# Optimization experiments

Hardware: AMD Instinct MI355X
Metric: run time of the kernel (lower is better)

## Reference

```python
import jax, jax.numpy as jnp
import numpy as np

N, C, H, W = 2, 256, 128, 128      # batch, fin=fout=fmiddle, feature resolution
SNC, NH, HS = 35, 128, 256         # semantic_nc, nhidden, raw segmap resolution
EPS = 1e-5                          # BatchNorm eps


def _conv(x, w, b, pad):
    y = jax.lax.conv_general_dilated(x, w, (1, 1), [(pad, pad), (pad, pad)],
                                     dimension_numbers=('NCHW', 'OIHW', 'NCHW'))
    return y + b[None, :, None, None]


def _bn(x, g, b):
    # training-mode BatchNorm2d: biased batch stats over (N, H, W)
    m = x.mean(axis=(0, 2, 3), keepdims=True)
    v = ((x - m) ** 2).mean(axis=(0, 2, 3), keepdims=True)
    return (x - m) * jax.lax.rsqrt(v + EPS) * g[None, :, None, None] + b[None, :, None, None]


def _depth_conv(x, w):
    # per-pixel dynamic 3x3 depthwise conv: unfold + multiply + reduce
    n, c, h, ww = x.shape
    xp = jnp.pad(x, ((0, 0), (0, 0), (1, 1), (1, 1)))
    patches = jnp.stack([xp[:, :, i:i + h, j:j + ww]
                         for i in range(3) for j in range(3)], axis=2)  # (N,C,9,H,W)
    return jnp.sum(patches * w.reshape(n, c, 9, h, ww), axis=2)


def _lrelu(x):
    return jnp.where(x >= 0, x, 0.2 * x)


def _branch(segmap, w1, b1, w2, b2):
    return _conv(jax.nn.relu(_conv(segmap, w1, b1, 1)), w2, b2, 1)


def _forward(x, seg, gw1_w1, gw1_b1, gw1_w2, gw1_b2, gw2_w1, gw2_b1, gw2_w2, gw2_b2,
             se1_w1, se1_b1, se1_w2, se1_b2, se2_w1, se2_b1, se2_w2, se2_b2,
             conv1_w, conv1_b, conv3_w, conv3_b, bn1_g, bn1_b, bn2_g, bn2_b):
    # F.interpolate(seg, size=(H, W), mode='nearest')
    ih = (jnp.arange(H) * seg.shape[2]) // H
    iw = (jnp.arange(W) * seg.shape[3]) // W
    segmap = seg[:, :, ih][:, :, :, iw]
    cw1 = _branch(segmap, gw1_w1, gw1_b1, gw1_w2, gw1_b2)                  # (N, C*9, H, W)
    cw2 = _branch(segmap, gw2_w1, gw2_b1, gw2_w2, gw2_b2)                  # (N, C*9, H, W)
    sw1 = jax.nn.sigmoid(_branch(segmap, se1_w1, se1_b1, se1_w2, se1_b2))  # (N, C, H, W)
    sw2 = jax.nn.sigmoid(_branch(segmap, se2_w1, se2_b1, se2_w2, se2_b2))  # (N, C, H, W)
    dx = _bn(x, bn1_g, bn1_b)
    dx = _depth_conv(dx, cw1)
    dx = _conv(dx, conv1_w, conv1_b, 0)
    dx = _lrelu(dx * sw1)
    dx = _bn(dx, bn2_g, bn2_b)
    dx = _depth_conv(dx, cw2)
    dx = _conv(dx, conv3_w, conv3_b, 0)
    dx = _lrelu(dx * sw2)
    return x + dx  # fin == fout -> identity shortcut


def setup_inputs() -> dict:
    key = jax.random.key(0)
    ks = jax.random.split(key, 22)
    def rn(i, shape, s=0.05):
        return jax.random.normal(ks[i], shape, jnp.float32) * s
    return {
        'x': jax.random.normal(ks[0], (N, C, H, W), jnp.float32),
        'seg': jax.random.uniform(ks[1], (N, SNC, HS, HS), jnp.float32),
        'gw1_w1': rn(2, (NH, SNC, 3, 3)), 'gw1_b1': rn(3, (NH,)),
        'gw1_w2': rn(4, (C * 9, NH, 3, 3)), 'gw1_b2': rn(5, (C * 9,)),
        'gw2_w1': rn(6, (NH, SNC, 3, 3)), 'gw2_b1': rn(7, (NH,)),
        'gw2_w2': rn(8, (C * 9, NH, 3, 3)), 'gw2_b2': rn(9, (C * 9,)),
        'se1_w1': rn(10, (NH, SNC, 3, 3)), 'se1_b1': rn(11, (NH,)),
        'se1_w2': rn(12, (C, NH, 3, 3)), 'se1_b2': rn(13, (C,)),
        'se2_w1': rn(14, (NH, SNC, 3, 3)), 'se2_b1': rn(15, (NH,)),
        'se2_w2': rn(16, (C, NH, 3, 3)), 'se2_b2': rn(17, (C,)),
        'conv1_w': rn(18, (C, C, 1, 1)), 'conv1_b': rn(19, (C,)),
        'conv3_w': rn(20, (C, C, 1, 1)), 'conv3_b': rn(21, (C,)),
        'bn1_g': jnp.ones((C,), jnp.float32), 'bn1_b': jnp.zeros((C,), jnp.float32),
        'bn2_g': jnp.ones((C,), jnp.float32), 'bn2_b': jnp.zeros((C,), jnp.float32),
    }


def reference(x, seg, gw1_w1, gw1_b1, gw1_w2, gw1_b2, gw2_w1, gw2_b1, gw2_w2, gw2_b2,
              se1_w1, se1_b1, se1_w2, se1_b2, se2_w1, se2_b1, se2_w2, se2_b2,
              conv1_w, conv1_b, conv3_w, conv3_b, bn1_g, bn1_b, bn2_g, bn2_b):
    return _forward(x, seg, gw1_w1, gw1_b1, gw1_w2, gw1_b2, gw2_w1, gw2_b1, gw2_w2, gw2_b2,
                    se1_w1, se1_b1, se1_w2, se1_b2, se2_w1, se2_b1, se2_w2, se2_b2,
                    conv1_w, conv1_b, conv3_w, conv3_b, bn1_g, bn1_b, bn2_g, bn2_b)
```

## Files before the change

kernel.cpp:

```cpp
#include <hip/hip_runtime.h>
#include <hip/hip_bf16.h>

typedef unsigned short u16;
typedef unsigned int u32;
typedef __attribute__((ext_vector_type(8))) short bf16x8;
typedef __attribute__((ext_vector_type(4))) float f32x4;
typedef __attribute__((address_space(3))) u32 lds_u32;
typedef const __attribute__((address_space(1))) u32 glb_u32;

#define H_ 128
#define W_ 128
#define PX 16384
#define PH 130

__device__ __forceinline__ float b2f(u16 h){ u32 u = ((u32)h)<<16; return __uint_as_float(u); }
__device__ __forceinline__ u16 f2b(float f){
  u32 u = __float_as_uint(f);
  u32 r = (u + 0x7fffu + ((u>>16)&1u)) >> 16;
  return (u16)r;
}
__device__ __forceinline__ float ldv(const void* p, long i, int m){
  return m ? ((const float*)p)[i] : b2f(((const u16*)p)[i]);
}
__device__ __forceinline__ void gload16(const u16* g, u16* l){
  __builtin_amdgcn_global_load_lds((glb_u32*)g, (lds_u32*)l, 16, 0, 0);
}

__global__ void k_detect(const u32* __restrict__ xw, u32* __restrict__ flag){
  __shared__ int cnt[256];
  const int t = threadIdx.x;
  int c = 0;
  #pragma unroll
  for (int i=0;i<4;i++){
    const u32 w = xw[t*4+i];
    const u32 e = ((w & 0xFFFFu) >> 7) & 0xFF;
    if (e >= 90 && e <= 140) c++;
  }
  cnt[t] = c; __syncthreads();
  for (int s=128;s>0;s>>=1){ if (t<s) cnt[t]+=cnt[t+s]; __syncthreads(); }
  if (t==0) flag[0] = (cnt[0] < 512) ? 1u : 0u;
}

__global__ void k_zpad(u16* __restrict__ h1t){
  const int p = blockIdx.x;
  u16* base = h1t + (long)p*2163200L;
  const int t = threadIdx.x;
  const int4 z = make_int4(0,0,0,0);
  for (int idx=t; idx<8256; idx+=256){
    long off;
    if (idx < 2080)       off = (long)idx*8;
    else if (idx < 4160)  off = 2146560L + (long)(idx-2080)*8;
    else if (idx < 6208){ const int r = 1 + (idx-4160)/16, w = (idx-4160)%16;
                          off = (long)r*16640 + w*8; }
    else {                const int r = 1 + (idx-6208)/16, w = (idx-6208)%16;
                          off = (long)r*16640 + 16512 + w*8; }
    *(int4*)(base + off) = z;
  }
}

template<int CIN, int NTAPS, int EPI>
__global__ __launch_bounds__(256, 2)
void k_convgemm(const u16* __restrict__ inp, const u16* __restrict__ wp,
                const u16* __restrict__ bias, const u16* __restrict__ swp,
                u16* __restrict__ outp, int nbco,
                long in_br, long w_br, int bias_br, long out_br,
                long in_n, int in_row, int in_x0,
                long out_n, long out_y, int out_px, int out_x0,
                long sw_n, int sw_y,
                const void* __restrict__ xres, const u32* __restrict__ flagp,
                void* __restrict__ outF, float* __restrict__ partp)
{
  __shared__ u16 ls[17408];
  u16* lsA = ls;
  u16* lsB = ls + 8192;

  const int bx  = blockIdx.x;
  const int y   = (NTAPS==9) ? (((bx&7)<<4) | (bx>>3)) : bx;
  const int br  = blockIdx.y / nbco;
  const int cb  = blockIdx.y - br*nbco;
  const int n   = blockIdx.z;
  const int tid = threadIdx.x;
  const int wave = tid >> 6, lane = tid & 63;
  const int l16 = lane & 15, lg = lane >> 4;
  const int chw = (wave >> 1) * 64;
  const int phw = (wave & 1) * 64;

  const u16* inb   = inp + (long)br*in_br + (long)n*in_n + in_x0 + (long)y*in_row;
  const u16* wb    = wp  + (long)br*w_br + (long)cb*128*(NTAPS*CIN);
  const u16* biasb = bias + (long)br*bias_br + cb*128;
  u16* outb = outp + (long)br*out_br + (long)n*out_n + out_x0 + (long)y*out_y;

  f32x4 acc[4][4];
  #pragma unroll
  for (int m=0;m<4;m++)
    #pragma unroll
    for (int q=0;q<4;q++) acc[m][q] = (f32x4){0.f,0.f,0.f,0.f};

  const int NSTEP = NTAPS*(CIN/64);
  for (int step=0; step<NSTEP; ++step){
    const int tap = step/(CIN/64);
    const int k0  = (step - tap*(CIN/64))*64;
    const int dy = (NTAPS==1)?0:(tap/3-1);
    const int dx = (NTAPS==1)?0:(tap%3-1);
    const u16* wsrc = wb  + tap*CIN + k0;
    const u16* bsrc = inb + (long)dy*in_row + dx*CIN + k0;
    #pragma unroll
    for (int i=0;i<4;i++){
      const int idx = (wave*4+i)*64 + lane;
      const int r = idx>>3, c = idx&7;
      const int cc = c ^ (r&7);
      gload16(wsrc + (long)r*(NTAPS*CIN) + cc*8, lsA + (wave*4+i)*512);
    }
    #pragma unroll
    for (int i=0;i<4;i++){
      const int idx = (wave*4+i)*64 + lane;
      const int r = idx>>3, c = idx&7;
      const int cc = c ^ (r&7);
      gload16(bsrc + (long)r*CIN + cc*8, lsB + (wave*4+i)*512);
    }
    __syncthreads();
    #pragma unroll
    for (int kk=0;kk<2;kk++){
      bf16x8 af[4], bfr[4];
      const int kc = kk*4 + lg;
      #pragma unroll
      for (int m=0;m<4;m++){
        const int r = chw + m*16 + l16;
        af[m] = *(const bf16x8*)(lsA + r*64 + ((kc ^ (r&7))<<3));
      }
      #pragma unroll
      for (int q=0;q<4;q++){
        const int r = phw + q*16 + l16;
        bfr[q] = *(const bf16x8*)(lsB + r*64 + ((kc ^ (r&7))<<3));
      }
      #pragma unroll
      for (int m=0;m<4;m++)
        #pragma unroll
        for (int q=0;q<4;q++)
          acc[m][q] = __builtin_amdgcn_mfma_f32_16x16x32_bf16(af[m], bfr[q], acc[m][q], 0,0,0);
    }
    __syncthreads();
  }

  #pragma unroll
  for (int m=0;m<4;m++){
    const int co = chw + m*16 + lg*4;
    const ushort4 bb = *(const ushort4*)(biasb + co);
    const float bv0=b2f(bb.x), bv1=b2f(bb.y), bv2=b2f(bb.z), bv3=b2f(bb.w);
    #pragma unroll
    for (int q=0;q<4;q++){
      const int px = phw + q*16 + l16;
      float v0 = acc[m][q][0] + bv0;
      float v1 = acc[m][q][1] + bv1;
      float v2 = acc[m][q][2] + bv2;
      float v3 = acc[m][q][3] + bv3;
      if (EPI==1){
        v0=fmaxf(v0,0.f); v1=fmaxf(v1,0.f); v2=fmaxf(v2,0.f); v3=fmaxf(v3,0.f);
      } else if (EPI==2){
        v0 = 1.f/(1.f+__expf(-v0)); v1 = 1.f/(1.f+__expf(-v1));
        v2 = 1.f/(1.f+__expf(-v2)); v3 = 1.f/(1.f+__expf(-v3));
      } else if (EPI==3 || EPI==4){
        const ushort4 sv = *(const ushort4*)(swp + (long)n*sw_n + (long)y*sw_y + (long)px*256 + cb*128 + co);
        v0 *= b2f(sv.x); v1 *= b2f(sv.y); v2 *= b2f(sv.z); v3 *= b2f(sv.w);
        v0 = v0>=0.f? v0 : 0.2f*v0;  v1 = v1>=0.f? v1 : 0.2f*v1;
        v2 = v2>=0.f? v2 : 0.2f*v2;  v3 = v3>=0.f? v3 : 0.2f*v3;
      }
      ushort4 ov; ov.x=f2b(v0); ov.y=f2b(v1); ov.z=f2b(v2); ov.w=f2b(v3);
      *(ushort4*)(ls + px*136 + co) = ov;
    }
  }
  __syncthreads();
  if (EPI == 4){
    const int m2 = (int)flagp[0];
    const int co = tid>>1, hf2 = tid&1;
    const long xoff = (((long)n*256 + cb*128 + co)*H_ + y)*W_ + hf2*64;
    const u16* lrow = ls + (hf2*64)*136 + co;
    if (m2){
      const float* xf = (const float*)xres;
      float* of = (float*)outF;
      #pragma unroll
      for (int i=0;i<16;i++){
        const float4 xv = *(const float4*)(xf + xoff + i*4);
        float4 ov;
        ov.x = xv.x + b2f(lrow[(i*4+0)*136]);
        ov.y = xv.y + b2f(lrow[(i*4+1)*136]);
        ov.z = xv.z + b2f(lrow[(i*4+2)*136]);
        ov.w = xv.w + b2f(lrow[(i*4+3)*136]);
        *(float4*)(of + xoff + i*4) = ov;
      }
    } else {
      const u16* xu = (const u16*)xres;
      u16* ou = (u16*)outF;
      #pragma unroll
      for (int i=0;i<8;i++){
        const bf16x8 xv = *(const bf16x8*)(xu + xoff + i*8);
        bf16x8 ov;
        #pragma unroll
        for (int e=0;e<8;e++)
          ov[e] = (short)f2b(b2f((u16)xv[e]) + b2f(lrow[(i*8+e)*136]));
        *(bf16x8*)(ou + xoff + i*8) = ov;
      }
    }
  } else {
    const int row = tid>>1, hf = tid&1;
    u16* og = outb + (long)row*out_px + cb*128 + hf*64;
    #pragma unroll
    for (int i=0;i<8;i++)
      *(int4*)(og + i*8) = *(const int4*)(ls + row*136 + hf*64 + i*8);
    if (EPI == 3){
      if (tid < 128){
        const int co = tid;
        float s = 0.f, q = 0.f;
        for (int px=0; px<128; ++px){
          const float v = b2f(ls[px*136 + co]);
          s += v; q += v*v;
        }
        float* o = partp + (((long)n*128 + y)*256 + cb*128 + co)*2;
        o[0] = s; o[1] = q;
      }
    }
  }
}

__global__ __launch_bounds__(256, 2)
void k_convdw(const u16* __restrict__ h1,
              const u16* __restrict__ wp,
              const u16* __restrict__ bp,
              const u16* __restrict__ xh,
              const float2* __restrict__ ss,
              u16* __restrict__ dd)
{
  __shared__ u16 ls[19008];
  u16* lsA = ls;
  u16* lsB = ls + 9216;

  const int bx = blockIdx.x, mt = blockIdx.y, n = blockIdx.z;
  const int y = ((bx&7)<<4) | (bx>>3);
  const int tid = threadIdx.x;
  const int wave = tid >> 6, lane = tid & 63;
  const int l16 = lane & 15, lg = lane >> 4;
  const int wn = wave * 32;

  const u16* wb = wp + (long)mt*144*1152;

  f32x4 acc[9][2];
  #pragma unroll
  for (int m=0;m<9;m++){ acc[m][0]=(f32x4){0,0,0,0}; acc[m][1]=(f32x4){0,0,0,0}; }

  for (int s=0; s<18; ++s){
    const int tap = s >> 1;
    const int k0  = (s & 1) * 64;
    const int dy = tap/3 - 1, dx = tap%3 - 1;
    const u16* wsrc = wb + tap*128 + k0;
    const u16* bsrc = h1 + (((long)n*PH + (y+dy+1))*PH + (dx+1))*128 + k0;
    #pragma unroll
    for (int i=0;i<4;i++){
      const int g = i*256 + tid;
      const int r = g>>3, c = g&7, sp = c ^ (r&7);
      gload16(wsrc + (long)r*1152 + sp*8, lsA + g*8);
    }
    if (tid < 128){
      const int g = 1024 + tid;
      const int r = g>>3, c = g&7, sp = c ^ (r&7);
      gload16(wsrc + (long)r*1152 + sp*8, lsA + g*8);
    }
    #pragma unroll
    for (int i=0;i<4;i++){
      const int g = i*256 + tid;
      const int p = g>>3, c = g&7, sp = c ^ (p&7);
      gload16(bsrc + (long)p*128 + sp*8, lsB + g*8);
    }
    __syncthreads();
    #pragma unroll
    for (int kk=0;kk<2;kk++){
      const int kc = kk*4 + lg;
      bf16x8 bfr[2];
      #pragma unroll
      for (int q=0;q<2;q++){
        const int rb = wn + q*16 + l16;
        bfr[q] = *(const bf16x8*)(lsB + rb*64 + ((kc ^ (rb&7))<<3));
      }
      #pragma unroll
      for (int m=0;m<9;m++){
        const int ra = m*16 + l16;
        const bf16x8 a = *(const bf16x8*)(lsA + ra*64 + ((kc ^ (ra&7))<<3));
        acc[m][0] = __builtin_amdgcn_mfma_f32_16x16x32_bf16(a, bfr[0], acc[m][0], 0,0,0);
        acc[m][1] = __builtin_amdgcn_mfma_f32_16x16x32_bf16(a, bfr[1], acc[m][1], 0,0,0);
      }
    }
    __syncthreads();
  }

  u16* ct = ls;
  #pragma unroll
  for (int m=0;m<9;m++){
    const int r0 = m*16 + lg*4;
    const ushort4 bb = *(const ushort4*)(bp + mt*144 + r0);
    const float bv0=b2f(bb.x), bv1=b2f(bb.y), bv2=b2f(bb.z), bv3=b2f(bb.w);
    #pragma unroll
    for (int q=0;q<2;q++){
      const int px = wn + q*16 + l16;
      ct[(r0+0)*132 + px] = f2b(acc[m][q][0] + bv0);
      ct[(r0+1)*132 + px] = f2b(acc[m][q][1] + bv1);
      ct[(r0+2)*132 + px] = f2b(acc[m][q][2] + bv2);
      ct[(r0+3)*132 + px] = f2b(acc[m][q][3] + bv3);
    }
  }
  __syncthreads();

  const int cl = tid & 15;
  const int c  = mt*16 + cl;
  const float2 sc = ss[c];
  const int xg = tid >> 4;
  #pragma unroll
  for (int i=0;i<8;i++){
    const int x = i*16 + xg;
    float a = 0.f;
    #pragma unroll
    for (int k=0;k<9;k++){
      const int ddy = k/3-1, ddx = k%3-1;
      const int gy = y+ddy, gx = x+ddx;
      if ((unsigned)gy < 128u && (unsigned)gx < 128u){
        const float xv = b2f(xh[(((long)n*PH + (gy+1))*PH + (gx+1))*256 + c]);
        const float w  = b2f(ct[(cl*9+k)*132 + x]);
        a += (xv*sc.x + sc.y) * w;
      }
    }
    dd[(((long)n*PX) + (long)y*W_ + x)*256 + c] = f2b(a);
  }
}

__global__ void k_bnstat2(const float* __restrict__ part, const void* __restrict__ g,
                          const void* __restrict__ b, const u32* __restrict__ flag,
                          float2* __restrict__ st)
{
  const int m = (int)flag[0];
  const int c = threadIdx.x;
  float s=0.f,q=0.f;
  for (int w=0;w<256;w++){ s += part[((long)w*256+c)*2]; q += part[((long)w*256+c)*2+1]; }
  const float mean = s*(1.f/32768.f);
  float v = q*(1.f/32768.f) - mean*mean;
  v = fmaxf(v, 0.f);
  const float sc = ldv(g,c,m) / sqrtf(v + 1e-5f);
  st[c] = make_float2(sc, ldv(b,c,m) - mean*sc);
}

__global__ void k_prep_w1(const void* a,const void* b,const void* c,const void* d,
                          const void* ba,const void* bb,const void* bc,const void* bd,
                          const u32* flag, u16* w1p, u16* bp1)
{
  const int m = (int)flag[0];
  const int idx = blockIdx.x*256 + threadIdx.x;
  if (idx < 294912){
    const int ci = idx & 63, r = (idx>>6)%9, co = (idx/576)%128, brn = idx/73728;
    const void* w = brn==0?a:brn==1?b:brn==2?c:d;
    u16 v = 0;
    if (ci < 35) v = f2b(ldv(w, ((long)co*35 + ci)*9 + r, m));
    w1p[idx] = v;
  }
  if (idx < 512){
    const int brn = idx>>7, co = idx&127;
    const void* bb2 = brn==0?ba:brn==1?bb:brn==2?bc:bd;
    bp1[idx] = f2b(ldv(bb2, co, m));
  }
}

__global__ void k_prep_gw(const void* __restrict__ w2, const void* __restrict__ b2,
                          const u32* __restrict__ flag,
                          u16* __restrict__ w2p, u16* __restrict__ bp)
{
  __shared__ u16 lt[2304];
  const int m = (int)flag[0];
  const int b = blockIdx.x;
  const int t = threadIdx.x;
  #pragma unroll
  for (int i=0;i<9;i++){
    const int g = i*256 + t;
    const long src = (long)b*2304 + g;
    const int lco = g/1152, rem = g - lco*1152;
    const int ci = rem/9, tap = rem - ci*9;
    lt[lco*1152 + tap*128 + ci] = f2b(ldv(w2, src, m));
  }
  __syncthreads();
  #pragma unroll
  for (int i=0;i<9;i++){
    const int g = i*256 + t;
    w2p[(long)b*2304 + g] = lt[g];
  }
  if (b < 9){
    const int bi = b*256 + t;
    if (bi < 2304) bp[bi] = f2b(ldv(b2, bi, m));
  }
}

__global__ void k_prep_se(const void* wa, const void* wb, const void* ba, const void* bb,
                          const u32* flag, u16* w2p, u16* bp)
{
  const int m = (int)flag[0];
  const int idx = blockIdx.x*256 + threadIdx.x;
  if (idx < 589824){
    const int ci = idx & 127, r = (idx>>7)%9, co = (idx/1152)%256, brn = idx/294912;
    const void* w = brn ? wb : wa;
    w2p[idx] = f2b(ldv(w, ((long)co*128 + ci)*9 + r, m));
  }
  if (idx < 512){
    const int brn = idx>>8, co = idx&255;
    bp[idx] = f2b(ldv(brn?bb:ba, co, m));
  }
}

__global__ void k_prep_c(const void* c1w, const void* c1b, const void* c3w, const void* c3b,
                         const u32* flag, u16* c1wp, u16* c1bp, u16* c3wp, u16* c3bp)
{
  const int m = (int)flag[0];
  const int idx = blockIdx.x*256 + threadIdx.x;
  if (idx < 65536){
    c1wp[idx] = f2b(ldv(c1w, idx, m));
    c3wp[idx] = f2b(ldv(c3w, idx, m));
  }
  if (idx < 256){
    c1bp[idx] = f2b(ldv(c1b, idx, m));
    c3bp[idx] = f2b(ldv(c3b, idx, m));
  }
}

__global__ __launch_bounds__(256)
void k_seg_t(const void* __restrict__ seg, const u32* __restrict__ flag,
             u16* __restrict__ segt)
{
  __shared__ u16 lt[8192];
  const int m = (int)flag[0];
  const int y = blockIdx.x, n = blockIdx.y, t = threadIdx.x;
  for (int i=t;i<8192;i+=256) lt[i]=0;
  __syncthreads();
  for (int idx=t; idx<128*35; idx+=256){
    const int x = idx/35, ci = idx - x*35;
    lt[x*64+ci] = f2b(ldv(seg, (((long)n*35 + ci)*256 + 2*y)*256 + 2*x, m));
  }
  __syncthreads();
  const int x = t>>1, hf = t&1;
  u16* o = segt + (((long)n*PH + (y+1))*PH + (x+1))*64 + hf*32;
  #pragma unroll
  for (int i=0;i<4;i++) *(int4*)(o + i*8) = *(const int4*)&lt[x*64 + hf*32 + i*8];
}

__global__ __launch_bounds__(256)
void k_x_t(const void* __restrict__ x, const u32* __restrict__ flag,
           u16* __restrict__ xt, float* __restrict__ part)
{
  __shared__ u16 lt[128*72];
  const int m = (int)flag[0];
  const int y = blockIdx.x, n = blockIdx.y, cb = blockIdx.z;
  const int t = threadIdx.x;
  const long base = ((long)n*256 + cb*64)*PX + (long)y*W_;
  if (m){
    const float* xf = (const float*)x + base;
    #pragma unroll
    for (int i=0;i<8;i++){
      const int q = i*256 + t;
      const int c = q>>5, x4 = (q&31)*4;
      const float4 v = *(const float4*)(xf + (long)c*PX + x4);
      lt[(x4+0)*72 + c] = f2b(v.x);
      lt[(x4+1)*72 + c] = f2b(v.y);
      lt[(x4+2)*72 + c] = f2b(v.z);
      lt[(x4+3)*72 + c] = f2b(v.w);
    }
  } else {
    const u16* xu = (const u16*)x + base;
    #pragma unroll
    for (int i=0;i<4;i++){
      const int q = i*256 + t;
      const int c = q>>4, x8 = (q&15)*8;
      const bf16x8 v = *(const bf16x8*)(xu + (long)c*PX + x8);
      #pragma unroll
      for (int e=0;e<8;e++) lt[(x8+e)*72 + c] = (u16)v[e];
    }
  }
  __syncthreads();
  const int xx = t>>1, hf = t&1;
  u16* o = xt + (((long)n*PH + (y+1))*PH + (xx+1))*256 + cb*64 + hf*32;
  #pragma unroll
  for (int i=0;i<4;i++) *(int4*)(o+i*8) = *(const int4*)&lt[xx*72 + hf*32 + i*8];
  if (t < 64){
    float s = 0.f, q = 0.f;
    for (int xi=0; xi<128; ++xi){
      const float v = b2f(lt[xi*72 + t]);
      s += v; q += v*v;
    }
    float* op = part + (((long)n*128 + y)*256 + cb*64 + t)*2;
    op[0] = s; op[1] = q;
  }
}

extern "C" void kernel_launch(void* const* d_in, const int* in_sizes, int n_in,
                              void* d_out, int out_size, void* d_ws, size_t ws_size,
                              hipStream_t stream)
{
  (void)in_sizes; (void)n_in; (void)out_size; (void)ws_size;
  const void* x      = d_in[0];
  const void* seg    = d_in[1];
  const void* gw1_w1 = d_in[2];
  const void* gw1_b1 = d_in[3];
  const void* gw1_w2 = d_in[4];
  const void* gw1_b2 = d_in[5];
  const void* gw2_w1 = d_in[6];
  const void* gw2_b1 = d_in[7];
  const void* gw2_w2 = d_in[8];
  const void* gw2_b2 = d_in[9];
  const void* se1_w1 = d_in[10];
  const void* se1_b1 = d_in[11];
  const void* se1_w2 = d_in[12];
  const void* se1_b2 = d_in[13];
  const void* se2_w1 = d_in[14];
  const void* se2_b1 = d_in[15];
  const void* se2_w2 = d_in[16];
  const void* se2_b2 = d_in[17];
  const void* c1w = d_in[18];
  const void* c1b = d_in[19];
  const void* c3w = d_in[20];
  const void* c3b = d_in[21];
  const void* bn1g = d_in[22];
  const void* bn1b = d_in[23];
  const void* bn2g = d_in[24];
  const void* bn2b = d_in[25];
  u16* ws = (u16*)d_ws;

  u16* segt  = ws;
  u16* xt    = ws + 2163200L;
  u16* t1    = xt;
  u16* dd    = ws + 10816000L;
  u16* sw1   = ws + 19204608L;
  u16* sw2   = ws + 27593216L;
  u16* w1p   = ws + 35981824L;
  u16* bp1   = ws + 36276736L;
  u16* w2pg1 = ws + 36277248L;
  u16* w2pg2 = ws + 38931456L;
  u16* bpg   = ws + 41585664L;
  u16* w2ps  = ws + 41590272L;
  u16* bps   = ws + 42180096L;
  u16* c1wp  = ws + 42180608L;
  u16* c1bp  = ws + 42246144L;
  u16* c3wp  = ws + 42246400L;
  u16* c3bp  = ws + 42311936L;
  float*  part = (float*)(ws + 42312192L);
  float2* st1  = (float2*)(ws + 42574336L);
  float2* st2  = (float2*)(ws + 42575360L);
  u32*    flag = (u32*)(ws + 42576384L);
  u16* h1t   = ws + 42576512L;

  hipMemsetAsync(segt, 0, 4326400ULL, stream);
  k_zpad<<<dim3(8),256,0,stream>>>(h1t);

  k_detect<<<dim3(1),256,0,stream>>>((const u32*)x, flag);
  k_prep_w1<<<dim3(1152),256,0,stream>>>(gw1_w1,gw2_w1,se1_w1,se2_w1,
                                         gw1_b1,gw2_b1,se1_b1,se2_b1, flag, w1p, bp1);
  k_prep_gw<<<dim3(1152),256,0,stream>>>(gw1_w2, gw1_b2, flag, w2pg1, bpg);
  k_prep_gw<<<dim3(1152),256,0,stream>>>(gw2_w2, gw2_b2, flag, w2pg2, bpg+2304);
  k_prep_se<<<dim3(2304),256,0,stream>>>(se1_w2, se2_w2, se1_b2, se2_b2, flag, w2ps, bps);
  k_prep_c<<<dim3(256),256,0,stream>>>(c1w, c1b, c3w, c3b, flag, c1wp, c1bp, c3wp, c3bp);
  k_seg_t<<<dim3(128,2),256,0,stream>>>(seg, flag, segt);
  k_x_t<<<dim3(128,2,4),256,0,stream>>>(x, flag, xt, part);

  k_convgemm<64,9,1><<<dim3(128,4,2),256,0,stream>>>(
      segt, w1p, bp1, nullptr, h1t, 1,
      0L, 73728L, 128, 4326400L,
      1081600L, 8320, 8384,
      2163200L, 16640L, 128, 16768, 0L, 0,
      nullptr, nullptr, nullptr, nullptr);

  k_convgemm<128,9,2><<<dim3(128,4,2),256,0,stream>>>(
      h1t + 2*4326400L, w2ps, bps, nullptr, sw1, 2,
      4326400L, 294912L, 256, 8388608L,
      2163200L, 16640, 16768,
      4194304L, 32768L, 256, 0, 0L, 0,
      nullptr, nullptr, nullptr, nullptr);

  k_bnstat2<<<dim3(1),256,0,stream>>>(part, bn1g, bn1b, flag, st1);

  k_convdw<<<dim3(128,16,2),256,0,stream>>>(h1t, w2pg1, bpg, xt, st1, dd);

  k_convgemm<256,1,3><<<dim3(128,2,2),256,0,stream>>>(
      dd, c1wp, c1bp, sw1, t1, 2,
      0L, 0L, 0, 0L,
      4194304L, 32768, 0,
      4326400L, 33280L, 256, 33536, 4194304L, 32768,
      nullptr, nullptr, nullptr, part);

  k_bnstat2<<<dim3(1),256,0,stream>>>(part, bn2g, bn2b, flag, st2);

  k_convdw<<<dim3(128,16,2),256,0,stream>>>(h1t + 4326400L, w2pg2, bpg+2304, t1, st2, dd);

  k_convgemm<256,1,4><<<dim3(128,2,2),256,0,stream>>>(
      dd, c3wp, c3bp, sw2, dd, 2,
      0L, 0L, 0, 0L,
      4194304L, 32768, 0,
      0L, 0L, 256, 0, 4194304L, 32768,
      x, flag, d_out, nullptr);
}
```

Baseline: 680.4 us.

## Stage x halo tile in LDS, transpose BN partials, coalesce SE weight prep

```diff
diff --git a/kernel.cpp b/kernel.cpp
--- a/kernel.cpp
+++ b/kernel.cpp
@@ -215,8 +215,9 @@
           const float v = b2f(ls[px*136 + co]);
           s += v; q += v*v;
         }
-        float* o = partp + (((long)n*128 + y)*256 + cb*128 + co)*2;
-        o[0] = s; o[1] = q;
+        const int cidx = cb*128 + co, w = n*128 + y;
+        partp[(long)cidx*256 + w] = s;
+        partp[65536L + (long)cidx*256 + w] = q;
       }
     }
   }
@@ -230,9 +231,10 @@
               const float2* __restrict__ ss,
               u16* __restrict__ dd)
 {
-  __shared__ u16 ls[19008];
+  __shared__ u16 ls[25248];
   u16* lsA = ls;
   u16* lsB = ls + 9216;
+  u16* xtile = ls + 19008;
 
   const int bx = blockIdx.x, mt = blockIdx.y, n = blockIdx.z;
   const int y = ((bx&7)<<4) | (bx>>3);
@@ -243,6 +245,19 @@
 
   const u16* wb = wp + (long)mt*144*1152;
 
+  {
+    const u16* xb = xh + ((long)n*PH + y)*PH*256 + mt*16;
+    #pragma unroll
+    for (int i=0;i<4;i++){
+      const int q = i*256 + tid;
+      if (q < 780){
+        const int h = q & 1, pos = q >> 1;
+        const int r = pos/130, xx = pos - r*130;
+        gload16(xb + ((long)r*PH + xx)*256 + h*8, xtile + q*8);
+      }
+    }
+  }
+
   f32x4 acc[9][2];
   #pragma unroll
   for (int m=0;m<9;m++){ acc[m][0]=(f32x4){0,0,0,0}; acc[m][1]=(f32x4){0,0,0,0}; }
@@ -321,7 +336,7 @@
       const int ddy = k/3-1, ddx = k%3-1;
       const int gy = y+ddy, gx = x+ddx;
       if ((unsigned)gy < 128u && (unsigned)gx < 128u){
-        const float xv = b2f(xh[(((long)n*PH + (gy+1))*PH + (gx+1))*256 + c]);
+        const float xv = b2f(xtile[((ddy+1)*130 + (gx+1))*16 + cl]);
         const float w  = b2f(ct[(cl*9+k)*132 + x]);
         a += (xv*sc.x + sc.y) * w;
       }
@@ -337,7 +352,7 @@
   const int m = (int)flag[0];
   const int c = threadIdx.x;
   float s=0.f,q=0.f;
-  for (int w=0;w<256;w++){ s += part[((long)w*256+c)*2]; q += part[((long)w*256+c)*2+1]; }
+  for (int w=0;w<256;w++){ s += part[(long)c*256 + w]; q += part[65536L + (long)c*256 + w]; }
   const float mean = s*(1.f/32768.f);
   float v = q*(1.f/32768.f) - mean*mean;
   v = fmaxf(v, 0.f);
@@ -396,17 +411,28 @@
 __global__ void k_prep_se(const void* wa, const void* wb, const void* ba, const void* bb,
                           const u32* flag, u16* w2p, u16* bp)
 {
+  __shared__ u16 lt[2304];
   const int m = (int)flag[0];
-  const int idx = blockIdx.x*256 + threadIdx.x;
-  if (idx < 589824){
-    const int ci = idx & 127, r = (idx>>7)%9, co = (idx/1152)%256, brn = idx/294912;
-    const void* w = brn ? wb : wa;
-    w2p[idx] = f2b(ldv(w, ((long)co*128 + ci)*9 + r, m));
-  }
-  if (idx < 512){
-    const int brn = idx>>8, co = idx&255;
-    bp[idx] = f2b(ldv(brn?bb:ba, co, m));
-  }
+  const int b = blockIdx.x;
+  const int brn = b >> 7;
+  const void* w = brn ? wb : wa;
+  const int t = threadIdx.x;
+  #pragma unroll
+  for (int i=0;i<9;i++){
+    const int g = i*256 + t;
+    const long src = (long)(b&127)*2304 + g;
+    const int lco = g/1152, rem = g - lco*1152;
+    const int ci = rem/9, tap = rem - ci*9;
+    lt[lco*1152 + tap*128 + ci] = f2b(ldv(w, src, m));
+  }
+  __syncthreads();
+  #pragma unroll
+  for (int i=0;i<9;i++){
+    const int g = i*256 + t;
+    w2p[(long)b*2304 + g] = lt[g];
+  }
+  if ((b & 127) == 0)
+    bp[brn*256 + t] = f2b(ldv(brn?bb:ba, t, m));
 }
 
 __global__ void k_prep_c(const void* c1w, const void* c1b, const void* c3w, const void* c3b,
@@ -487,8 +513,9 @@
       const float v = b2f(lt[xi*72 + t]);
       s += v; q += v*v;
     }
-    float* op = part + (((long)n*128 + y)*256 + cb*64 + t)*2;
-    op[0] = s; op[1] = q;
+    const int cidx = cb*64 + t, w = n*128 + y;
+    part[(long)cidx*256 + w] = s;
+    part[65536L + (long)cidx*256 + w] = q;
   }
 }
 
@@ -556,7 +583,7 @@
                                          gw1_b1,gw2_b1,se1_b1,se2_b1, flag, w1p, bp1);
   k_prep_gw<<<dim3(1152),256,0,stream>>>(gw1_w2, gw1_b2, flag, w2pg1, bpg);
   k_prep_gw<<<dim3(1152),256,0,stream>>>(gw2_w2, gw2_b2, flag, w2pg2, bpg+2304);
-  k_prep_se<<<dim3(2304),256,0,stream>>>(se1_w2, se2_w2, se1_b2, se2_b2, flag, w2ps, bps);
+  k_prep_se<<<dim3(256),256,0,stream>>>(se1_w2, se2_w2, se1_b2, se2_b2, flag, w2ps, bps);
   k_prep_c<<<dim3(256),256,0,stream>>>(c1w, c1b, c3w, c3b, flag, c1wp, c1bp, c3wp, c3bp);
   k_seg_t<<<dim3(128,2),256,0,stream>>>(seg, flag, segt);
   k_x_t<<<dim3(128,2,4),256,0,stream>>>(x, flag, xt, part);
```

Measured after the change: 596.3 us. 1.14x faster.
